# Optimization experiments

Measured on AMD Instinct MI355X. Metric: run time of the kernel, lower is better.

The kernel has to match this reference:

```python
import jax, jax.numpy as jnp
import numpy as np

L, V, D, H, F, S = 6, 32000, 768, 12, 3072, 1024
B, T = 2, 1024
DK = D // H
EPS = 1e-5  # torch LayerNorm default


def _ln(x, w, b):
    m = x.mean(-1, keepdims=True)
    v = ((x - m) ** 2).mean(-1, keepdims=True)
    return (x - m) / jnp.sqrt(v + EPS) * w + b


def setup_inputs() -> dict:
    key = jax.random.key(0)
    ks = jax.random.split(key, 16)
    n = lambda k, shape: jax.random.normal(k, shape, jnp.float32) * 0.02
    return {
        "x": jax.random.randint(ks[0], (B, T), 0, V),
        "tok_emb": n(ks[1], (V, D)),
        "pos_emb": n(ks[2], (S, D)),
        "ln1_w": jnp.ones((L, D), jnp.float32), "ln1_b": jnp.zeros((L, D), jnp.float32),
        "wq": n(ks[3], (L, D, D)), "bq": jnp.zeros((L, D), jnp.float32),
        "wk": n(ks[4], (L, D, D)), "bk": jnp.zeros((L, D), jnp.float32),
        "wv": n(ks[5], (L, D, D)), "bv": jnp.zeros((L, D), jnp.float32),
        "wo": n(ks[6], (L, D, D)), "bo": jnp.zeros((L, D), jnp.float32),
        "ln2_w": jnp.ones((L, D), jnp.float32), "ln2_b": jnp.zeros((L, D), jnp.float32),
        "w1": n(ks[7], (L, F, D)), "b1": jnp.zeros((L, F), jnp.float32),
        "w2": n(ks[8], (L, D, F)), "b2": jnp.zeros((L, D), jnp.float32),
        "lnf_w": jnp.ones((D,), jnp.float32), "lnf_b": jnp.zeros((D,), jnp.float32),
        "head_w": n(ks[9], (V, D)),
    }


def reference(x, tok_emb, pos_emb, ln1_w, ln1_b, wq, bq, wk, bk, wv, bv, wo, bo,
              ln2_w, ln2_b, w1, b1, w2, b2, lnf_w, lnf_b, head_w):
    Bx, Tx = x.shape
    h = tok_emb[x] + pos_emb[:Tx]                     # [B,T,D]
    causal = jnp.triu(jnp.ones((Tx, Tx), bool), 1)    # True above diagonal
    scale = 1.0 / np.sqrt(DK)
    for i in range(L):
        a = _ln(h, ln1_w[i], ln1_b[i])
        q = (a @ wq[i].T + bq[i]).reshape(Bx, Tx, H, DK).transpose(0, 2, 1, 3)
        k = (a @ wk[i].T + bk[i]).reshape(Bx, Tx, H, DK).transpose(0, 2, 1, 3)
        v = (a @ wv[i].T + bv[i]).reshape(Bx, Tx, H, DK).transpose(0, 2, 1, 3)
        scores = jnp.einsum("bhtd,bhsd->bhts", q, k) * scale  # [B,H,T,T]
        scores = jnp.where(causal, -jnp.inf, scores)
        attn = jax.nn.softmax(scores, axis=-1)
        ctx = jnp.einsum("bhts,bhsd->bhtd", attn, v)
        ctx = ctx.transpose(0, 2, 1, 3).reshape(Bx, Tx, D)
        h = h + ctx @ wo[i].T + bo[i]
        f = _ln(h, ln2_w[i], ln2_b[i])
        h = h + jax.nn.relu(f @ w1[i].T + b1[i]) @ w2[i].T + b2[i]
    h = _ln(h, lnf_w, lnf_b)
    return h @ head_w.T                               # [B,T,V] logits
```

## Files before the change

kernel.cpp:

```cpp
#include <hip/hip_runtime.h>

typedef unsigned short u16;
typedef __bf16 bf16x8 __attribute__((ext_vector_type(8)));
typedef float f32x4 __attribute__((ext_vector_type(4)));
typedef float f32x4v __attribute__((ext_vector_type(4)));
typedef u16 u16x4 __attribute__((ext_vector_type(4)));

__device__ __forceinline__ float bf2f(u16 u) {
    unsigned x = ((unsigned)u) << 16;
    return __builtin_bit_cast(float, x);
}
__device__ __forceinline__ u16 f2bf(float f) {
    unsigned x = __builtin_bit_cast(unsigned, f);
    unsigned r = (x + 0x7FFFu + ((x >> 16) & 1u)) >> 16;
    return (u16)r;
}

__global__ __launch_bounds__(256) void cvt_kernel(const float* __restrict__ in,
                                                  u16* __restrict__ out, long n) {
    for (long i = (long)blockIdx.x * 1024 + (long)threadIdx.x * 4; i < n;
         i += (long)gridDim.x * 1024) {
        f32x4v v = *(const f32x4v*)(in + i);
        u16x4 o;
        o.x = f2bf(v.x); o.y = f2bf(v.y); o.z = f2bf(v.z); o.w = f2bf(v.w);
        *(u16x4*)(out + i) = o;
    }
}

__global__ __launch_bounds__(256) void bias_fuse_kernel(const float* __restrict__ bq,
                                                        const float* __restrict__ bk,
                                                        const float* __restrict__ bv,
                                                        float* __restrict__ dst) {
    int i = blockIdx.x * 256 + threadIdx.x;
    if (i < 6 * 768) {
        int l = i / 768, j = i % 768;
        dst[l * 2304 + j] = bq[i];
        dst[l * 2304 + 768 + j] = bk[i];
        dst[l * 2304 + 1536 + j] = bv[i];
    }
}

__global__ __launch_bounds__(256) void embed_kernel(const int* __restrict__ x,
                                                    const float* __restrict__ tok,
                                                    const float* __restrict__ pos,
                                                    float* __restrict__ h) {
    int row = blockIdx.x;
    int t = row & 1023;
    long id = x[row];
    const float* te = tok + id * 768L;
    const float* pe = pos + (long)t * 768L;
    float* o = h + (long)row * 768L;
    for (int d = threadIdx.x; d < 768; d += 256) o[d] = te[d] + pe[d];
}

__global__ __launch_bounds__(256) void ln_kernel(const float* __restrict__ x,
                                                 const float* __restrict__ w,
                                                 const float* __restrict__ b,
                                                 u16* __restrict__ out) {
    __shared__ float red[4];
    int row = blockIdx.x;
    const float* xr = x + (long)row * 768L;
    int tid = threadIdx.x, lane = tid & 63, wid = tid >> 6;
    float v0 = xr[tid], v1 = xr[tid + 256], v2 = xr[tid + 512];
    float s = v0 + v1 + v2;
    for (int o = 32; o; o >>= 1) s += __shfl_xor(s, o);
    if (lane == 0) red[wid] = s;
    __syncthreads();
    float mean = (red[0] + red[1] + red[2] + red[3]) * (1.f / 768.f);
    __syncthreads();
    float d0 = v0 - mean, d1 = v1 - mean, d2 = v2 - mean;
    float q = d0 * d0 + d1 * d1 + d2 * d2;
    for (int o = 32; o; o >>= 1) q += __shfl_xor(q, o);
    if (lane == 0) red[wid] = q;
    __syncthreads();
    float var = (red[0] + red[1] + red[2] + red[3]) * (1.f / 768.f);
    float rstd = rsqrtf(var + 1e-5f);
    u16* orow = out + (long)row * 768L;
    orow[tid]       = f2bf(d0 * rstd * w[tid]       + b[tid]);
    orow[tid + 256] = f2bf(d1 * rstd * w[tid + 256] + b[tid + 256]);
    orow[tid + 512] = f2bf(d2 * rstd * w[tid + 512] + b[tid + 512]);
}

__global__ __launch_bounds__(256) void redln_kernel(
    const float* __restrict__ part, long pstride, int S,
    const float* __restrict__ bias, float* __restrict__ h,
    const float* __restrict__ w, const float* __restrict__ b,
    u16* __restrict__ out) {
    __shared__ float red[4];
    int row = blockIdx.x;
    int tid = threadIdx.x, lane = tid & 63, wid = tid >> 6;
    long base = (long)row * 768;
    float v[3];
#pragma unroll
    for (int e3 = 0; e3 < 3; e3++) {
        int e = tid + 256 * e3;
        float x = h[base + e] + bias[e];
        for (int s = 0; s < S; s++) x += part[(long)s * pstride + base + e];
        v[e3] = x;
        h[base + e] = x;
    }
    float s = v[0] + v[1] + v[2];
    for (int o = 32; o; o >>= 1) s += __shfl_xor(s, o);
    if (lane == 0) red[wid] = s;
    __syncthreads();
    float mean = (red[0] + red[1] + red[2] + red[3]) * (1.f / 768.f);
    __syncthreads();
    float d0 = v[0] - mean, d1 = v[1] - mean, d2 = v[2] - mean;
    float q = d0 * d0 + d1 * d1 + d2 * d2;
    for (int o = 32; o; o >>= 1) q += __shfl_xor(q, o);
    if (lane == 0) red[wid] = q;
    __syncthreads();
    float var = (red[0] + red[1] + red[2] + red[3]) * (1.f / 768.f);
    float rstd = rsqrtf(var + 1e-5f);
    u16* orow = out + base;
    orow[tid]       = f2bf(d0 * rstd * w[tid]       + b[tid]);
    orow[tid + 256] = f2bf(d1 * rstd * w[tid + 256] + b[tid + 256]);
    orow[tid + 512] = f2bf(d2 * rstd * w[tid + 512] + b[tid + 512]);
}

__global__ __launch_bounds__(256) void flash_kernel(
    const u16* __restrict__ qkv,
    const u16* __restrict__ vT,
    u16* __restrict__ ctx) {
    int z = blockIdx.z;
    int zb = z / 12, zh = z - zb * 12;
    int qt = (int)gridDim.x - 1 - (int)blockIdx.x;
    int q0 = qt * 64;
    int tid = threadIdx.x, lane = tid & 63, wid = tid >> 6;
    int rA = lane & 15, sA = lane >> 4;

    const u16* Qbase = qkv + (long)zb * 1024 * 2304 + zh * 64;
    const u16* Kbase = Qbase + 768;
    const u16* Vbase = vT + (long)z * 64 * 1024;

    __shared__ u16 Ks[64 * 64];
    __shared__ u16 Vs[64 * 64];
    __shared__ u16 Ps[4][16 * 64];

    bf16x8 aq[2];
    {
        const u16* qrow = Qbase + (long)(q0 + wid * 16 + rA) * 2304;
        aq[0] = *(const bf16x8*)(qrow + sA * 8);
        aq[1] = *(const bf16x8*)(qrow + 32 + sA * 8);
    }

    float m[4], l[4];
    f32x4 acc_o[4];
#pragma unroll
    for (int j = 0; j < 4; j++) { m[j] = -1e30f; l[j] = 0.f; }
#pragma unroll
    for (int nf = 0; nf < 4; nf++) acc_o[nf] = 0.f;

    int grow0 = q0 + wid * 16 + sA * 4;
    int nkv = qt + 1;
    for (int t = 0; t < nkv; ++t) {
        int kv0 = t * 64;
#pragma unroll
        for (int c0 = 0; c0 < 512; c0 += 256) {
            int c = c0 + tid;
            int row = c >> 3, half = (c >> 2) & 1, sl = c & 3;
            int ks = sl ^ ((row >> 1) & 3);
            __builtin_amdgcn_global_load_lds(
                (const __attribute__((address_space(1))) unsigned*)(Kbase + (long)(kv0 + row) * 2304 + half * 32 + ks * 8),
                (__attribute__((address_space(3))) unsigned*)(Ks + c * 8), 16, 0, 0);
        }
#pragma unroll
        for (int c0 = 0; c0 < 512; c0 += 256) {
            int c = c0 + tid;
            int row = c >> 3, half = (c >> 2) & 1, sl = c & 3;
            int ks = sl ^ ((row >> 1) & 3);
            __builtin_amdgcn_global_load_lds(
                (const __attribute__((address_space(1))) unsigned*)(Vbase + (long)row * 1024 + kv0 + half * 32 + ks * 8),
                (__attribute__((address_space(3))) unsigned*)(Vs + c * 8), 16, 0, 0);
        }
        __syncthreads();

        f32x4 s[4];
#pragma unroll
        for (int nf = 0; nf < 4; nf++) s[nf] = 0.f;
#pragma unroll
        for (int h = 0; h < 2; h++)
#pragma unroll
            for (int nf = 0; nf < 4; nf++) {
                int row = nf * 16 + rA;
                bf16x8 bk_ = *(const bf16x8*)(Ks + row * 64 + h * 32 + ((sA ^ ((row >> 1) & 3))) * 8);
                s[nf] = __builtin_amdgcn_mfma_f32_16x16x32_bf16(aq[h], bk_, s[nf], 0, 0, 0);
            }
#pragma unroll
        for (int nf = 0; nf < 4; nf++) {
            int col = kv0 + nf * 16 + rA;
#pragma unroll
            for (int j = 0; j < 4; j++)
                s[nf][j] = (col <= grow0 + j) ? s[nf][j] * 0.125f : -1e30f;
        }
        float pm[4];
#pragma unroll
        for (int j = 0; j < 4; j++) {
            float v = fmaxf(fmaxf(s[0][j], s[1][j]), fmaxf(s[2][j], s[3][j]));
#pragma unroll
            for (int o = 1; o < 16; o <<= 1) v = fmaxf(v, __shfl_xor(v, o));
            pm[j] = v;
        }
        float esc[4];
#pragma unroll
        for (int j = 0; j < 4; j++) {
            float mn = fmaxf(m[j], pm[j]);
            esc[j] = __expf(m[j] - mn);
            m[j] = mn;
        }
        float ts[4] = {0.f, 0.f, 0.f, 0.f};
#pragma unroll
        for (int nf = 0; nf < 4; nf++) {
            int c = nf * 16 + rA;
            int half = c >> 5, ch = (c >> 3) & 3, e = c & 7;
#pragma unroll
            for (int j = 0; j < 4; j++) {
                float p = __expf(s[nf][j] - m[j]);
                ts[j] += p;
                int r = sA * 4 + j;
                Ps[wid][r * 64 + half * 32 + (ch ^ ((r >> 1) & 3)) * 8 + e] = f2bf(p);
            }
        }
#pragma unroll
        for (int j = 0; j < 4; j++) {
            float v = ts[j];
#pragma unroll
            for (int o = 1; o < 16; o <<= 1) v += __shfl_xor(v, o);
            l[j] = l[j] * esc[j] + v;
        }
#pragma unroll
        for (int nf = 0; nf < 4; nf++)
#pragma unroll
            for (int j = 0; j < 4; j++) acc_o[nf][j] *= esc[j];

#pragma unroll
        for (int h = 0; h < 2; h++) {
            bf16x8 ap = *(const bf16x8*)(Ps[wid] + rA * 64 + h * 32 + ((sA ^ ((rA >> 1) & 3))) * 8);
#pragma unroll
            for (int nf = 0; nf < 4; nf++) {
                int row = nf * 16 + rA;
                bf16x8 bv_ = *(const bf16x8*)(Vs + row * 64 + h * 32 + ((sA ^ ((row >> 1) & 3))) * 8);
                acc_o[nf] = __builtin_amdgcn_mfma_f32_16x16x32_bf16(ap, bv_, acc_o[nf], 0, 0, 0);
            }
        }
        __syncthreads();
    }

    float inv[4];
#pragma unroll
    for (int j = 0; j < 4; j++) inv[j] = 1.f / l[j];
    u16* crow = ctx + ((long)zb * 1024 + q0 + wid * 16) * 768 + zh * 64;
#pragma unroll
    for (int nf = 0; nf < 4; nf++)
#pragma unroll
        for (int j = 0; j < 4; j++)
            crow[(long)(sA * 4 + j) * 768 + nf * 16 + rA] = f2bf(acc_o[nf][j] * inv[j]);
}

template <int BM, int BN, int EPI, int SK>
__global__ __launch_bounds__(256) void gemm3_kernel(
    const u16* __restrict__ A, int lda,
    const u16* __restrict__ Bm, int ldb,
    void* __restrict__ Cv, int ldc,
    const float* __restrict__ bias, int Kslice, int gm,
    u16* __restrict__ aux, int gemmBlocks, long partStride,
    const float* __restrict__ c0src, u16* __restrict__ c0dst, long c0n,
    const float* __restrict__ c1src, u16* __restrict__ c1dst, long c1n) {
    constexpr int BK = 32;
    int flat = blockIdx.x;
    int tid = threadIdx.x;
    if (flat >= gemmBlocks) {
        int P = (int)gridDim.x - gemmBlocks;
        int pid = flat - gemmBlocks;
        int P0 = P >> 1;
        const float* src; u16* dst; long n; long b0; long nb;
        if (pid < P0) { src = c0src; dst = c0dst; n = c0n; b0 = pid; nb = P0; }
        else { src = c1src; dst = c1dst; n = c1n; b0 = pid - P0; nb = P - P0; }
        if (src) {
            for (long i = b0 * 1024 + (long)tid * 4; i < n; i += nb * 1024) {
                f32x4v v = *(const f32x4v*)(src + i);
                u16x4 o;
                o.x = f2bf(v.x); o.y = f2bf(v.y); o.z = f2bf(v.z); o.w = f2bf(v.w);
                *(u16x4*)(dst + i) = o;
            }
        }
        return;
    }
    int nwg = gemmBlocks;
    int qq = nwg >> 3, rr = nwg & 7;
    int xcd = flat & 7, wi = flat >> 3;
    int swz = (xcd < rr) ? (xcd * (qq + 1) + wi) : (rr * (qq + 1) + (xcd - rr) * qq + wi);
    int slice = 0, wblk = swz;
    if (SK > 1) { int nbs = nwg / SK; slice = swz / nbs; wblk = swz - slice * nbs; }
    int ntile = wblk / gm, mt = wblk - ntile * gm;
    int bm0 = mt * BM, bn0 = ntile * BN;
    long koff = (long)slice * Kslice;
    const u16* Ab = A + (long)bm0 * lda + koff;
    const u16* Bb = Bm + (long)bn0 * ldb + koff;

    __shared__ u16 As[2][BM * BK];
    __shared__ u16 Bs[2][BN * BK];

    int lane = tid & 63, wid = tid >> 6;
    constexpr int WM = BM / 2, WN = BN / 2, MR = WM / 16, NR = WN / 16;
    int wm0 = (wid >> 1) * WM, wn0 = (wid & 1) * WN;

    f32x4 acc[MR][NR];
#pragma unroll
    for (int mi = 0; mi < MR; mi++)
#pragma unroll
        for (int ni = 0; ni < NR; ni++) acc[mi][ni] = 0.f;

    int nt = Kslice / BK;

    auto stage = [&](int buf, int k0) {
        constexpr int CA = BM * 4;
#pragma unroll
        for (int c0 = 0; c0 < CA; c0 += 256) {
            int c = c0 + tid;
            int row = c >> 2, sl = c & 3;
            int ks = sl ^ ((row >> 1) & 3);
            __builtin_amdgcn_global_load_lds(
                (const __attribute__((address_space(1))) unsigned*)(Ab + (long)row * lda + k0 + ks * 8),
                (__attribute__((address_space(3))) unsigned*)(As[buf] + c * 8), 16, 0, 0);
        }
        constexpr int CB = BN * 4;
#pragma unroll
        for (int c0 = 0; c0 < CB; c0 += 256) {
            int c = c0 + tid;
            int row = c >> 2, sl = c & 3;
            int ks = sl ^ ((row >> 1) & 3);
            __builtin_amdgcn_global_load_lds(
                (const __attribute__((address_space(1))) unsigned*)(Bb + (long)row * ldb + k0 + ks * 8),
                (__attribute__((address_space(3))) unsigned*)(Bs[buf] + c * 8), 16, 0, 0);
        }
    };

    stage(0, 0);
    __syncthreads();
    int cur = 0;
    int rA = lane & 15, sA = lane >> 4;
    int sswz = (sA ^ ((rA >> 1) & 3)) * 8;
    for (int t = 0; t < nt; ++t) {
        if (t + 1 < nt) stage(cur ^ 1, (t + 1) * BK);
        bf16x8 af[MR], bfr[NR];
#pragma unroll
        for (int mi = 0; mi < MR; mi++)
            af[mi] = *(const bf16x8*)(As[cur] + (wm0 + mi * 16 + rA) * BK + sswz);
#pragma unroll
        for (int ni = 0; ni < NR; ni++)
            bfr[ni] = *(const bf16x8*)(Bs[cur] + (wn0 + ni * 16 + rA) * BK + sswz);
#pragma unroll
        for (int mi = 0; mi < MR; mi++)
#pragma unroll
            for (int ni = 0; ni < NR; ni++)
                acc[mi][ni] = __builtin_amdgcn_mfma_f32_16x16x32_bf16(
                    af[mi], bfr[ni], acc[mi][ni], 0, 0, 0);
        __syncthreads();
        cur ^= 1;
    }

#pragma unroll
    for (int mi = 0; mi < MR; mi++)
#pragma unroll
        for (int ni = 0; ni < NR; ni++) {
            int gmb = bm0 + wm0 + mi * 16 + ((lane >> 4) << 2);
            int gn = bn0 + wn0 + ni * 16 + (lane & 15);
            if (EPI == 6) {
                if (gn < 1536) {
#pragma unroll
                    for (int j = 0; j < 4; j++)
                        ((u16*)Cv)[(long)(gmb + j) * ldc + gn] =
                            f2bf(acc[mi][ni][j] + bias[gn]);
                } else {
                    u16x4 o;
#pragma unroll
                    for (int j = 0; j < 4; j++) o[j] = f2bf(acc[mi][ni][j] + bias[gn]);
                    int hh = (gn - 1536) >> 6, dk = gn & 63;
                    long off = ((long)((gmb >> 10) * 12 + hh) * 64 + dk) * 1024 + (gmb & 1023);
                    *(u16x4*)(aux + off) = o;
                }
            } else {
#pragma unroll
                for (int j = 0; j < 4; j++) {
                    float v = acc[mi][ni][j];
                    long idx = (long)(gmb + j) * ldc + gn;
                    if (EPI == 2) ((u16*)Cv)[idx] = f2bf(fmaxf(v + bias[gn], 0.f));
                    else ((float*)Cv)[(long)slice * partStride + idx] = v;
                }
            }
        }
}

extern "C" void kernel_launch(void* const* d_in, const int* in_sizes, int n_in,
                              void* d_out, int out_size, void* d_ws, size_t ws_size,
                              hipStream_t stream) {
    const int L = 6, D = 768, F = 3072, T = 1024, V = 32000;
    const int M = 2048;
    const int* x = (const int*)d_in[0];
    const float* tok = (const float*)d_in[1];
    const float* pos = (const float*)d_in[2];
    const float* ln1w = (const float*)d_in[3];
    const float* ln1b = (const float*)d_in[4];
    const float* wq = (const float*)d_in[5];
    const float* bq = (const float*)d_in[6];
    const float* wk = (const float*)d_in[7];
    const float* bk = (const float*)d_in[8];
    const float* wv = (const float*)d_in[9];
    const float* bv = (const float*)d_in[10];
    const float* wo = (const float*)d_in[11];
    const float* bo = (const float*)d_in[12];
    const float* ln2w = (const float*)d_in[13];
    const float* ln2b = (const float*)d_in[14];
    const float* w1 = (const float*)d_in[15];
    const float* b1 = (const float*)d_in[16];
    const float* w2 = (const float*)d_in[17];
    const float* b2 = (const float*)d_in[18];
    const float* lnfw = (const float*)d_in[19];
    const float* lnfb = (const float*)d_in[20];
    const float* headw = (const float*)d_in[21];

    char* p = (char*)d_ws;
    auto alloc = [&](size_t bytes) {
        char* r = p;
        p += (bytes + 255) & ~(size_t)255;
        return r;
    };
    const long DD = (long)D * D, FD = (long)F * D;
    const long PS = (long)M * D;
    const long HC = 2048000;
    u16* qkvw_b = (u16*)alloc(L * 3 * DD * 2);
    u16* wo_b = (u16*)alloc(L * DD * 2);
    u16* w1_b = (u16*)alloc(L * FD * 2);
    u16* w2_b = (u16*)alloc(L * FD * 2);
    u16* hw_b = (u16*)alloc((long)V * D * 2);
    float* qkvbias = (float*)alloc(L * 2304 * 4);
    float* h = (float*)alloc((long)M * D * 4);
    u16* a = (u16*)alloc((long)M * D * 2);
    u16* qkvb = (u16*)alloc((long)M * 2304 * 2);
    u16* vT = (u16*)alloc(24L * 64 * T * 2);
    u16* ctxb = (u16*)alloc((long)M * D * 2);
    u16* f1 = (u16*)alloc((long)M * F * 2);
    float* part = (float*)alloc(4L * PS * 4);

    auto cvt = [&](const float* src, u16* dst, long n) {
        long blocks = (n + 1023) / 1024;
        if (blocks > 4096) blocks = 4096;
        cvt_kernel<<<dim3((unsigned)blocks), 256, 0, stream>>>(src, dst, n);
    };
    cvt(wq, qkvw_b, DD);
    cvt(wk, qkvw_b + DD, DD);
    cvt(wv, qkvw_b + 2 * DD, DD);
    cvt(wo, wo_b, DD);
    cvt(w1, w1_b, FD);
    cvt(w2, w2_b, FD);
    bias_fuse_kernel<<<dim3(18), 256, 0, stream>>>(bq, bk, bv, qkvbias);
    embed_kernel<<<dim3(M), 256, 0, stream>>>(x, tok, pos, h);
    ln_kernel<<<dim3(M), 256, 0, stream>>>(h, ln1w, ln1b, a);

    for (int i = 0; i < L; i++) {
        int nx = i + 1;
        bool hn = nx < L;
        {
            int pg = hn ? 128 : 0;
            gemm3_kernel<128, 128, 6, 1><<<dim3(288 + pg), 256, 0, stream>>>(
                a, D, qkvw_b + i * 3 * DD, D, qkvb, 2304, qkvbias + i * 2304,
                D, 16, vT, 288, 0,
                hn ? wq + nx * DD : nullptr, qkvw_b + nx * 3 * DD, DD,
                hn ? wk + nx * DD : nullptr, qkvw_b + nx * 3 * DD + DD, DD);
        }
        flash_kernel<<<dim3(16, 1, 24), 256, 0, stream>>>(qkvb, vT, ctxb);
        gemm3_kernel<64, 128, 5, 2><<<dim3(384 + 128), 256, 0, stream>>>(
            ctxb, D, wo_b + i * DD, D, part, D, nullptr, 384, 32, nullptr,
            384, PS,
            hn ? wv + nx * DD : nullptr, qkvw_b + nx * 3 * DD + 2 * DD, DD,
            hn ? wo + nx * DD : nullptr, wo_b + nx * DD, DD);
        redln_kernel<<<dim3(M), 256, 0, stream>>>(
            part, PS, 2, bo + i * D, h, ln2w + i * D, ln2b + i * D, a);
        gemm3_kernel<128, 128, 2, 1><<<dim3(384 + 128), 256, 0, stream>>>(
            a, D, w1_b + i * FD, D, f1, F, b1 + i * F, D, 16, nullptr, 384, 0,
            hn ? w1 + nx * FD : nullptr, w1_b + nx * FD, FD,
            headw + (2 * i) * HC, hw_b + (2 * i) * HC, HC);
        gemm3_kernel<64, 128, 5, 4><<<dim3(768 + 128), 256, 0, stream>>>(
            f1, F, w2_b + i * FD, F, part, D, nullptr, 768, 32, nullptr,
            768, PS,
            hn ? w2 + nx * FD : nullptr, w2_b + nx * FD, FD,
            headw + (2 * i + 1) * HC, hw_b + (2 * i + 1) * HC, HC);
        redln_kernel<<<dim3(M), 256, 0, stream>>>(
            part, PS, 4, b2 + i * D, h,
            hn ? ln1w + nx * D : lnfw, hn ? ln1b + nx * D : lnfb, a);
    }
    gemm3_kernel<128, 128, 5, 1><<<dim3(4000), 256, 0, stream>>>(
        a, D, hw_b, D, d_out, V, nullptr, D, 16, nullptr, 4000, 0,
        nullptr, nullptr, 0, nullptr, nullptr, 0);
}
```

Before: 1.114 ms.

## Add BK=64 GEMM tiles, smaller QKV/FFN1 tiles, vectorized redln, MFMA priority

The GEMM kernel is templated on the K-tile size. BK=64 gets an 8-way swizzle and two MFMA k-steps per stage, halving the number of barrier and staging iterations. The QKV and FFN1 GEMMs move to 64x128 tiles, which doubles their block counts for better CU fill. The residual-reduce LayerNorm kernel now uses 192 threads with float4 loads and stores. The flash kernel raises wave priority around its MFMA sections. The trade-off is more LDS per block for BK=64 and more A-tile reloads with the smaller M tile.

```diff
diff --git a/kernel.cpp b/kernel.cpp
--- a/kernel.cpp
+++ b/kernel.cpp
@@ -81,41 +81,41 @@
     orow[tid + 512] = f2bf(d2 * rstd * w[tid + 512] + b[tid + 512]);
 }
 
-__global__ __launch_bounds__(256) void redln_kernel(
+__global__ __launch_bounds__(192) void redln_kernel(
     const float* __restrict__ part, long pstride, int S,
     const float* __restrict__ bias, float* __restrict__ h,
     const float* __restrict__ w, const float* __restrict__ b,
     u16* __restrict__ out) {
-    __shared__ float red[4];
+    __shared__ float red[3];
     int row = blockIdx.x;
     int tid = threadIdx.x, lane = tid & 63, wid = tid >> 6;
-    long base = (long)row * 768;
-    float v[3];
-#pragma unroll
-    for (int e3 = 0; e3 < 3; e3++) {
-        int e = tid + 256 * e3;
-        float x = h[base + e] + bias[e];
-        for (int s = 0; s < S; s++) x += part[(long)s * pstride + base + e];
-        v[e3] = x;
-        h[base + e] = x;
-    }
-    float s = v[0] + v[1] + v[2];
+    long base = (long)row * 768 + tid * 4;
+    f32x4v x = *(const f32x4v*)(h + base);
+    f32x4v bb = *(const f32x4v*)(bias + tid * 4);
+    x += bb;
+    for (int s = 0; s < S; s++) x += *(const f32x4v*)(part + (long)s * pstride + base);
+    *(f32x4v*)(h + base) = x;
+    float s = x.x + x.y + x.z + x.w;
     for (int o = 32; o; o >>= 1) s += __shfl_xor(s, o);
     if (lane == 0) red[wid] = s;
     __syncthreads();
-    float mean = (red[0] + red[1] + red[2] + red[3]) * (1.f / 768.f);
-    __syncthreads();
-    float d0 = v[0] - mean, d1 = v[1] - mean, d2 = v[2] - mean;
-    float q = d0 * d0 + d1 * d1 + d2 * d2;
+    float mean = (red[0] + red[1] + red[2]) * (1.f / 768.f);
+    __syncthreads();
+    f32x4v d = x - mean;
+    float q = d.x * d.x + d.y * d.y + d.z * d.z + d.w * d.w;
     for (int o = 32; o; o >>= 1) q += __shfl_xor(q, o);
     if (lane == 0) red[wid] = q;
     __syncthreads();
-    float var = (red[0] + red[1] + red[2] + red[3]) * (1.f / 768.f);
+    float var = (red[0] + red[1] + red[2]) * (1.f / 768.f);
     float rstd = rsqrtf(var + 1e-5f);
-    u16* orow = out + base;
-    orow[tid]       = f2bf(d0 * rstd * w[tid]       + b[tid]);
-    orow[tid + 256] = f2bf(d1 * rstd * w[tid + 256] + b[tid + 256]);
-    orow[tid + 512] = f2bf(d2 * rstd * w[tid + 512] + b[tid + 512]);
+    f32x4v wv = *(const f32x4v*)(w + tid * 4);
+    f32x4v bv = *(const f32x4v*)(b + tid * 4);
+    u16x4 o;
+    o.x = f2bf(d.x * rstd * wv.x + bv.x);
+    o.y = f2bf(d.y * rstd * wv.y + bv.y);
+    o.z = f2bf(d.z * rstd * wv.z + bv.z);
+    o.w = f2bf(d.w * rstd * wv.w + bv.w);
+    *(u16x4*)(out + base) = o;
 }
 
 __global__ __launch_bounds__(256) void flash_kernel(
@@ -178,6 +178,7 @@
         f32x4 s[4];
 #pragma unroll
         for (int nf = 0; nf < 4; nf++) s[nf] = 0.f;
+        __builtin_amdgcn_s_setprio(1);
 #pragma unroll
         for (int h = 0; h < 2; h++)
 #pragma unroll
@@ -186,6 +187,7 @@
                 bf16x8 bk_ = *(const bf16x8*)(Ks + row * 64 + h * 32 + ((sA ^ ((row >> 1) & 3))) * 8);
                 s[nf] = __builtin_amdgcn_mfma_f32_16x16x32_bf16(aq[h], bk_, s[nf], 0, 0, 0);
             }
+        __builtin_amdgcn_s_setprio(0);
 #pragma unroll
         for (int nf = 0; nf < 4; nf++) {
             int col = kv0 + nf * 16 + rA;
@@ -233,6 +235,7 @@
 #pragma unroll
             for (int j = 0; j < 4; j++) acc_o[nf][j] *= esc[j];
 
+        __builtin_amdgcn_s_setprio(1);
 #pragma unroll
         for (int h = 0; h < 2; h++) {
             bf16x8 ap = *(const bf16x8*)(Ps[wid] + rA * 64 + h * 32 + ((sA ^ ((rA >> 1) & 3))) * 8);
@@ -243,6 +246,7 @@
                 acc_o[nf] = __builtin_amdgcn_mfma_f32_16x16x32_bf16(ap, bv_, acc_o[nf], 0, 0, 0);
             }
         }
+        __builtin_amdgcn_s_setprio(0);
         __syncthreads();
     }
 
@@ -257,8 +261,8 @@
             crow[(long)(sA * 4 + j) * 768 + nf * 16 + rA] = f2bf(acc_o[nf][j] * inv[j]);
 }
 
-template <int BM, int BN, int EPI, int SK>
-__global__ __launch_bounds__(256) void gemm3_kernel(
+template <int BM, int BN, int BK, int EPI, int SK>
+__global__ __launch_bounds__(256) void gemm8_kernel(
     const u16* __restrict__ A, int lda,
     const u16* __restrict__ Bm, int ldb,
     void* __restrict__ Cv, int ldc,
@@ -266,7 +270,8 @@
     u16* __restrict__ aux, int gemmBlocks, long partStride,
     const float* __restrict__ c0src, u16* __restrict__ c0dst, long c0n,
     const float* __restrict__ c1src, u16* __restrict__ c1dst, long c1n) {
-    constexpr int BK = 32;
+    constexpr int CPR = BK / 8;
+    constexpr int KH = BK / 32;
     int flat = blockIdx.x;
     int tid = threadIdx.x;
     if (flat >= gemmBlocks) {
@@ -313,23 +318,25 @@
 
     int nt = Kslice / BK;
 
+    auto key = [](int row) { return (BK == 32) ? ((row >> 1) & 3) : (row & 7); };
+
     auto stage = [&](int buf, int k0) {
-        constexpr int CA = BM * 4;
+        constexpr int CA = BM * CPR;
 #pragma unroll
         for (int c0 = 0; c0 < CA; c0 += 256) {
             int c = c0 + tid;
-            int row = c >> 2, sl = c & 3;
-            int ks = sl ^ ((row >> 1) & 3);
+            int row = c / CPR, sl = c & (CPR - 1);
+            int ks = sl ^ key(row);
             __builtin_amdgcn_global_load_lds(
                 (const __attribute__((address_space(1))) unsigned*)(Ab + (long)row * lda + k0 + ks * 8),
                 (__attribute__((address_space(3))) unsigned*)(As[buf] + c * 8), 16, 0, 0);
         }
-        constexpr int CB = BN * 4;
+        constexpr int CB = BN * CPR;
 #pragma unroll
         for (int c0 = 0; c0 < CB; c0 += 256) {
             int c = c0 + tid;
-            int row = c >> 2, sl = c & 3;
-            int ks = sl ^ ((row >> 1) & 3);
+            int row = c / CPR, sl = c & (CPR - 1);
+            int ks = sl ^ key(row);
             __builtin_amdgcn_global_load_lds(
                 (const __attribute__((address_space(1))) unsigned*)(Bb + (long)row * ldb + k0 + ks * 8),
                 (__attribute__((address_space(3))) unsigned*)(Bs[buf] + c * 8), 16, 0, 0);
@@ -340,22 +347,31 @@
     __syncthreads();
     int cur = 0;
     int rA = lane & 15, sA = lane >> 4;
-    int sswz = (sA ^ ((rA >> 1) & 3)) * 8;
     for (int t = 0; t < nt; ++t) {
         if (t + 1 < nt) stage(cur ^ 1, (t + 1) * BK);
-        bf16x8 af[MR], bfr[NR];
-#pragma unroll
-        for (int mi = 0; mi < MR; mi++)
-            af[mi] = *(const bf16x8*)(As[cur] + (wm0 + mi * 16 + rA) * BK + sswz);
-#pragma unroll
-        for (int ni = 0; ni < NR; ni++)
-            bfr[ni] = *(const bf16x8*)(Bs[cur] + (wn0 + ni * 16 + rA) * BK + sswz);
-#pragma unroll
-        for (int mi = 0; mi < MR; mi++)
-#pragma unroll
-            for (int ni = 0; ni < NR; ni++)
-                acc[mi][ni] = __builtin_amdgcn_mfma_f32_16x16x32_bf16(
-                    af[mi], bfr[ni], acc[mi][ni], 0, 0, 0);
+        bf16x8 af[MR][KH], bfr[NR][KH];
+#pragma unroll
+        for (int mi = 0; mi < MR; mi++) {
+            int row = wm0 + mi * 16 + rA;
+#pragma unroll
+            for (int h = 0; h < KH; h++)
+                af[mi][h] = *(const bf16x8*)(As[cur] + row * BK + (((h << 2) + sA) ^ key(row)) * 8);
+        }
+#pragma unroll
+        for (int ni = 0; ni < NR; ni++) {
+            int row = wn0 + ni * 16 + rA;
+#pragma unroll
+            for (int h = 0; h < KH; h++)
+                bfr[ni][h] = *(const bf16x8*)(Bs[cur] + row * BK + (((h << 2) + sA) ^ key(row)) * 8);
+        }
+#pragma unroll
+        for (int h = 0; h < KH; h++)
+#pragma unroll
+            for (int mi = 0; mi < MR; mi++)
+#pragma unroll
+                for (int ni = 0; ni < NR; ni++)
+                    acc[mi][ni] = __builtin_amdgcn_mfma_f32_16x16x32_bf16(
+                        af[mi][h], bfr[ni][h], acc[mi][ni], 0, 0, 0);
         __syncthreads();
         cur ^= 1;
     }
@@ -463,34 +479,34 @@
         bool hn = nx < L;
         {
             int pg = hn ? 128 : 0;
-            gemm3_kernel<128, 128, 6, 1><<<dim3(288 + pg), 256, 0, stream>>>(
+            gemm8_kernel<64, 128, 64, 6, 1><<<dim3(576 + pg), 256, 0, stream>>>(
                 a, D, qkvw_b + i * 3 * DD, D, qkvb, 2304, qkvbias + i * 2304,
-                D, 16, vT, 288, 0,
+                D, 32, vT, 576, 0,
                 hn ? wq + nx * DD : nullptr, qkvw_b + nx * 3 * DD, DD,
                 hn ? wk + nx * DD : nullptr, qkvw_b + nx * 3 * DD + DD, DD);
         }
         flash_kernel<<<dim3(16, 1, 24), 256, 0, stream>>>(qkvb, vT, ctxb);
-        gemm3_kernel<64, 128, 5, 2><<<dim3(384 + 128), 256, 0, stream>>>(
+        gemm8_kernel<64, 128, 64, 5, 2><<<dim3(384 + 128), 256, 0, stream>>>(
             ctxb, D, wo_b + i * DD, D, part, D, nullptr, 384, 32, nullptr,
             384, PS,
             hn ? wv + nx * DD : nullptr, qkvw_b + nx * 3 * DD + 2 * DD, DD,
             hn ? wo + nx * DD : nullptr, wo_b + nx * DD, DD);
-        redln_kernel<<<dim3(M), 256, 0, stream>>>(
+        redln_kernel<<<dim3(M), 192, 0, stream>>>(
             part, PS, 2, bo + i * D, h, ln2w + i * D, ln2b + i * D, a);
-        gemm3_kernel<128, 128, 2, 1><<<dim3(384 + 128), 256, 0, stream>>>(
-            a, D, w1_b + i * FD, D, f1, F, b1 + i * F, D, 16, nullptr, 384, 0,
+        gemm8_kernel<64, 128, 64, 2, 1><<<dim3(768 + 128), 256, 0, stream>>>(
+            a, D, w1_b + i * FD, D, f1, F, b1 + i * F, D, 32, nullptr, 768, 0,
             hn ? w1 + nx * FD : nullptr, w1_b + nx * FD, FD,
             headw + (2 * i) * HC, hw_b + (2 * i) * HC, HC);
-        gemm3_kernel<64, 128, 5, 4><<<dim3(768 + 128), 256, 0, stream>>>(
+        gemm8_kernel<64, 128, 64, 5, 4><<<dim3(768 + 128), 256, 0, stream>>>(
             f1, F, w2_b + i * FD, F, part, D, nullptr, 768, 32, nullptr,
             768, PS,
             hn ? w2 + nx * FD : nullptr, w2_b + nx * FD, FD,
             headw + (2 * i + 1) * HC, hw_b + (2 * i + 1) * HC, HC);
-        redln_kernel<<<dim3(M), 256, 0, stream>>>(
+        redln_kernel<<<dim3(M), 192, 0, stream>>>(
             part, PS, 4, b2 + i * D, h,
             hn ? ln1w + nx * D : lnfw, hn ? ln1b + nx * D : lnfb, a);
     }
-    gemm3_kernel<128, 128, 5, 1><<<dim3(4000), 256, 0, stream>>>(
+    gemm8_kernel<128, 128, 32, 5, 1><<<dim3(4000), 256, 0, stream>>>(
         a, D, hw_b, D, d_out, V, nullptr, D, 16, nullptr, 4000, 0,
         nullptr, nullptr, 0, nullptr, nullptr, 0);
 }
```

Result: faster. 1.082 ms (-2.9%).
